# Kernel tuning notes

Hardware: AMD Instinct MI355X
Metric: run time of the kernel (lower is better)

## Reference

```python
import jax, jax.numpy as jnp
import numpy as np

NUM_USERS, NUM_ITEMS = 100000, 50000
N_NODES = NUM_USERS + NUM_ITEMS
N_EDGES = 4_000_000
H = 64
BATCH = 100000
MLP_HIDDEN = 32
N_LAYERS = 3


def setup_inputs() -> dict:
    key = jax.random.key(0)
    ks = jax.random.split(key, 12)
    return {
        "edge_index": jax.random.randint(ks[0], (2, N_EDGES), 0, N_NODES, dtype=jnp.int32),
        "user_ids": jax.random.randint(ks[1], (BATCH,), 0, NUM_USERS, dtype=jnp.int32),
        "item_ids": jax.random.randint(ks[2], (BATCH,), 0, NUM_ITEMS, dtype=jnp.int32),
        "user_emb": jax.random.normal(ks[3], (NUM_USERS, H), jnp.float32),
        "item_emb": jax.random.normal(ks[4], (NUM_ITEMS, H), jnp.float32),
        "Wl": jax.random.normal(ks[5], (N_LAYERS, H, H), jnp.float32) * (1.0 / jnp.sqrt(H)),
        "bl": jnp.zeros((N_LAYERS, H), jnp.float32),
        "Wr": jax.random.normal(ks[6], (N_LAYERS, H, H), jnp.float32) * (1.0 / jnp.sqrt(H)),
        "W1": jax.random.normal(ks[7], (2 * H, MLP_HIDDEN), jnp.float32) * (1.0 / jnp.sqrt(2.0 * H)),
        "b1": jnp.zeros((MLP_HIDDEN,), jnp.float32),
        "W2": jax.random.normal(ks[8], (MLP_HIDDEN, 1), jnp.float32) * (1.0 / jnp.sqrt(1.0 * MLP_HIDDEN)),
        "b2": jnp.zeros((1,), jnp.float32),
    }


def _sage_layer(x, src, dst, Wl_i, bl_i, Wr_i):
    # PyG SAGEConv, mean aggr: out = lin_l(mean_{j in N(i)} x_j) + lin_r(x_i)
    msg = x[src]                                                  # [E, H] gather
    summed = jax.ops.segment_sum(msg, dst, num_segments=N_NODES)  # [N, H] scatter-add
    cnt = jax.ops.segment_sum(jnp.ones((src.shape[0],), x.dtype), dst, num_segments=N_NODES)
    mean = summed / jnp.maximum(cnt, 1.0)[:, None]                # empty neighborhoods -> 0
    return mean @ Wl_i + bl_i + x @ Wr_i


def reference(edge_index, user_ids, item_ids, user_emb, item_emb, Wl, bl, Wr, W1, b1, W2, b2):
    src, dst = edge_index[0], edge_index[1]
    x = jnp.concatenate([user_emb, item_emb], axis=0)  # [N, H]
    for l in range(N_LAYERS):
        x = jax.nn.relu(_sage_layer(x, src, dst, Wl[l], bl[l], Wr[l]))
        # dropout is identity in eval mode
    ue = x[user_ids]                   # [B, H]
    ie = x[item_ids + NUM_USERS]       # [B, H]
    pair = jnp.concatenate([ue, ie], axis=-1)  # [B, 2H]
    h = jax.nn.relu(pair @ W1 + b1)
    rating = (h @ W2 + b2)[:, 0]
    return jnp.clip(rating, 1.0, 5.0)
```

## Files before the change

### kernel.cpp

```cpp
#include <hip/hip_runtime.h>
#include <hip/hip_bf16.h>

#define NUM_USERS 100000
#define NUM_ITEMS 50000
#define N_NODES   150000
#define N_EDGES   4000000
#define H         64
#define BATCH     100000
#define MLP_HIDDEN 32
#define NBUCK     586
#define BCAP      8192
#define ZROW      N_NODES

typedef unsigned short ushort_t;
typedef float f32x2 __attribute__((ext_vector_type(2)));

__device__ __forceinline__ ushort_t f2bf(float f) {
    unsigned u = __float_as_uint(f);
    u = u + 0x7FFFu + ((u >> 16) & 1u);
    return (ushort_t)(u >> 16);
}
__device__ __forceinline__ float bfLO(unsigned u) { return __uint_as_float(u << 16); }
__device__ __forceinline__ float bfHI(unsigned u) { return __uint_as_float(u & 0xFFFF0000u); }

__global__ __launch_bounds__(256) void init_kernel(const float* __restrict__ ue,
                                                   const float* __restrict__ ie,
                                                   ushort_t* __restrict__ xh) {
    int i = blockIdx.x * 256 + threadIdx.x;
    const int UN4 = NUM_USERS * H / 4;
    float4 v = (i < UN4) ? ((const float4*)ue)[i] : ((const float4*)ie)[i - UN4];
    uint2 p;
    p.x = (unsigned)f2bf(v.x) | ((unsigned)f2bf(v.y) << 16);
    p.y = (unsigned)f2bf(v.z) | ((unsigned)f2bf(v.w) << 16);
    ((uint2*)xh)[i] = p;
}

#define SCHUNK 4096
#define SPT    (SCHUNK / 256)
__global__ __launch_bounds__(256) void bucket_scatter_kernel(const int* __restrict__ src,
                                                             const int* __restrict__ dst,
                                                             int* __restrict__ bucketCnt,
                                                             int* __restrict__ ebuf) {
    __shared__ int      histL[NBUCK];
    __shared__ int      startL[NBUCK];
    __shared__ int      adjL[NBUCK];
    __shared__ int      curL[NBUCK];
    __shared__ unsigned staged[SCHUNK];
    __shared__ ushort_t sbuck[SCHUNK];

    int t = threadIdx.x;
    int base = blockIdx.x * SCHUNK;
    int nst = min(SCHUNK, N_EDGES - base);

    for (int i = t; i < NBUCK; i += 256) histL[i] = 0;
    __syncthreads();

    int myd[SPT], mys[SPT];
#pragma unroll
    for (int k = 0; k < SPT; ++k) {
        int e = base + k * 256 + t;
        int d = (e < N_EDGES) ? dst[e] : -1;
        mys[k] = (e < N_EDGES) ? src[e] : 0;
        myd[k] = d;
        if (d >= 0) atomicAdd(&histL[d >> 8], 1);
    }
    __syncthreads();

    if (t < 64) {
        const int CH = (NBUCK + 63) / 64;
        int s0 = t * CH;
        int s1 = min(s0 + CH, NBUCK);
        int s = 0;
        for (int i = s0; i < s1; ++i) s += histL[i];
        int v = s;
#pragma unroll
        for (int off = 1; off < 64; off <<= 1) {
            int u = __shfl_up(v, off, 64);
            if (t >= off) v += u;
        }
        int run = v - s;
        for (int i = s0; i < s1; ++i) {
            startL[i] = run;
            run += histL[i];
        }
    }
    __syncthreads();

    for (int b = t; b < NBUCK; b += 256) {
        int h = histL[b];
        int res = h ? (b * BCAP + atomicAdd(&bucketCnt[b], h)) : 0;
        adjL[b] = res - startL[b];
        curL[b] = startL[b];
    }
    __syncthreads();

#pragma unroll
    for (int k = 0; k < SPT; ++k) {
        int d = myd[k];
        if (d >= 0) {
            int b = d >> 8;
            int pos = atomicAdd(&curL[b], 1);
            staged[pos] = ((unsigned)mys[k] << 8) | (unsigned)(d & 255);
            sbuck[pos] = (ushort_t)b;
        }
    }
    __syncthreads();

    for (int i = t; i < nst; i += 256) {
        int b = sbuck[i];
        ebuf[adjL[b] + i] = (int)staged[i];
    }
}

__global__ __launch_bounds__(512) void bucket_build_kernel(const int* __restrict__ ebuf,
                                                           const int* __restrict__ bucketCnt,
                                                           int* __restrict__ deg,
                                                           int* __restrict__ offsets,
                                                           int* __restrict__ csr) {
    __shared__ int degL[256];
    __shared__ int scanL[256];
    __shared__ int curL[256];
    int t = threadIdx.x;
    int b = blockIdx.x;
    int nodeBase = b << 8;
    int start = b * BCAP;
    int cnt = bucketCnt[b];

    if (t < 256) degL[t] = 0;
    __syncthreads();
    for (int i = t; i < cnt; i += 512)
        atomicAdd(&degL[ebuf[start + i] & 255], 1);
    __syncthreads();

    int v  = (t < 256) ? degL[t] : 0;
    int vp = (v + 3) & ~3;
    if (t < 256) scanL[t] = vp;
    __syncthreads();
#pragma unroll
    for (int off = 1; off < 256; off <<= 1) {
        int u = (t >= off && t < 256) ? scanL[t - off] : 0;
        __syncthreads();
        if (t < 256) scanL[t] += u;
        __syncthreads();
    }

    int excl = 0;
    if (t < 256) {
        excl = scanL[t] - vp;
        int node = nodeBase + t;
        if (node < N_NODES) {
            deg[node] = v;
            offsets[node] = start + excl;
        }
        curL[t] = excl;
    }
    __syncthreads();

    for (int i = t; i < cnt; i += 512) {
        unsigned p = (unsigned)ebuf[start + i];
        int pos = atomicAdd(&curL[p & 255u], 1);
        csr[start + pos] = (int)(p >> 8);
    }
    __syncthreads();

    if (t < 256) {
        for (int i = excl + v; i < excl + vp; ++i) csr[start + i] = ZROW;
    }
}

__global__ __launch_bounds__(256, 8) void gather_mean_kernel(const ushort_t* __restrict__ xh,
                                                             ushort_t* __restrict__ mean_bf,
                                                             const int* __restrict__ offsets,
                                                             const int* __restrict__ deg,
                                                             const int* __restrict__ csr) {
    int slot = threadIdx.x >> 6;
    int lane = threadIdx.x & 63;
    int q    = lane >> 4;
    int fp   = lane & 15;
    int node = blockIdx.x * 4 + slot;

    int base = offsets[node];
    int cnt  = deg[node];
    int cnt4 = (cnt + 3) & ~3;
    const uint2* xr = (const uint2*)xh;

    float a0 = 0.f, a1 = 0.f, a2 = 0.f, a3 = 0.f;

    for (int c = 0; c < cnt4; c += 64) {
        int rem = cnt4 - c;
        int sid = (lane < rem) ? csr[base + c + lane] : ZROW;
        int nq = min(64, rem) >> 2;
#define PROC(JJ) { int s = __shfl(sid, 4 * (JJ) + q, 64);                 \
        uint2 u = xr[s * 16 + fp];                                        \
        a0 += bfLO(u.x); a1 += bfHI(u.x); a2 += bfLO(u.y); a3 += bfHI(u.y); }
        int j = 0;
        for (; j + 2 <= nq; j += 2) { PROC(j) PROC(j + 1) }
        for (; j < nq; ++j) { PROC(j) }
#undef PROC
    }

    a0 += __shfl_xor(a0, 16, 64); a1 += __shfl_xor(a1, 16, 64);
    a2 += __shfl_xor(a2, 16, 64); a3 += __shfl_xor(a3, 16, 64);
    a0 += __shfl_xor(a0, 32, 64); a1 += __shfl_xor(a1, 32, 64);
    a2 += __shfl_xor(a2, 32, 64); a3 += __shfl_xor(a3, 32, 64);

    if (lane < 16) {
        float rc = 1.0f / fmaxf((float)cnt, 1.0f);
        uint2 p;
        p.x = (unsigned)f2bf(a0 * rc) | ((unsigned)f2bf(a1 * rc) << 16);
        p.y = (unsigned)f2bf(a2 * rc) | ((unsigned)f2bf(a3 * rc) << 16);
        *(uint2*)&mean_bf[node * H + fp * 4] = p;
    }
}

__global__ __launch_bounds__(256) void transform_kernel(ushort_t* __restrict__ xh,
                                                        const ushort_t* __restrict__ mean_bf,
                                                        const float* __restrict__ Wl,
                                                        const float* __restrict__ bl,
                                                        const float* __restrict__ Wr) {
    __shared__ float    sWl[H * H];
    __shared__ float    sWr[H * H];
    __shared__ unsigned sMT[H / 2][128];
    __shared__ unsigned sXT[H / 2][128];

    int t = threadIdx.x;
    int node0 = blockIdx.x * 128;

    for (int i = t; i < H * H / 4; i += 256) {
        ((float4*)sWl)[i] = ((const float4*)Wl)[i];
        ((float4*)sWr)[i] = ((const float4*)Wr)[i];
    }
#pragma unroll
    for (int it = 0; it < 8; ++it) {
        int idx = it * 256 + t;
        int n = idx & 127;
        int qd = idx >> 7;
        int node = node0 + n;
        uint2 mu = make_uint2(0u, 0u);
        uint2 xu = make_uint2(0u, 0u);
        if (node < N_NODES) {
            mu = *(const uint2*)&mean_bf[node * H + qd * 4];
            xu = *(const uint2*)&xh[node * H + qd * 4];
        }
        sMT[qd * 2][n]     = mu.x;
        sMT[qd * 2 + 1][n] = mu.y;
        sXT[qd * 2][n]     = xu.x;
        sXT[qd * 2 + 1][n] = xu.y;
    }
    __syncthreads();

    int tx = t & 7;
    int ty = t >> 3;
    int nbase = node0 + ty * 4;

    f32x2 acc[4][4];
#pragma unroll
    for (int j = 0; j < 4; ++j)
#pragma unroll
        for (int p = 0; p < 4; ++p) acc[j][p] = (f32x2)(0.0f);

    for (int kp = 0; kp < H / 2; ++kp) {
        uint4 mu = *(const uint4*)&sMT[kp][ty * 4];
        uint4 xu = *(const uint4*)&sXT[kp][ty * 4];
        int k0 = kp * 2;
        float4 wl00 = *(const float4*)&sWl[k0 * H + tx * 8];
        float4 wl01 = *(const float4*)&sWl[k0 * H + tx * 8 + 4];
        float4 wr00 = *(const float4*)&sWr[k0 * H + tx * 8];
        float4 wr01 = *(const float4*)&sWr[k0 * H + tx * 8 + 4];
        float4 wl10 = *(const float4*)&sWl[(k0 + 1) * H + tx * 8];
        float4 wl11 = *(const float4*)&sWl[(k0 + 1) * H + tx * 8 + 4];
        float4 wr10 = *(const float4*)&sWr[(k0 + 1) * H + tx * 8];
        float4 wr11 = *(const float4*)&sWr[(k0 + 1) * H + tx * 8 + 4];
        f32x2 wl0p[4] = {{wl00.x, wl00.y}, {wl00.z, wl00.w}, {wl01.x, wl01.y}, {wl01.z, wl01.w}};
        f32x2 wr0p[4] = {{wr00.x, wr00.y}, {wr00.z, wr00.w}, {wr01.x, wr01.y}, {wr01.z, wr01.w}};
        f32x2 wl1p[4] = {{wl10.x, wl10.y}, {wl10.z, wl10.w}, {wl11.x, wl11.y}, {wl11.z, wl11.w}};
        f32x2 wr1p[4] = {{wr10.x, wr10.y}, {wr10.z, wr10.w}, {wr11.x, wr11.y}, {wr11.z, wr11.w}};
        const unsigned mua[4] = {mu.x, mu.y, mu.z, mu.w};
        const unsigned xua[4] = {xu.x, xu.y, xu.z, xu.w};
#pragma unroll
        for (int j = 0; j < 4; ++j) {
            f32x2 m0 = (f32x2)(bfLO(mua[j]));
            f32x2 m1 = (f32x2)(bfHI(mua[j]));
            f32x2 x0 = (f32x2)(bfLO(xua[j]));
            f32x2 x1 = (f32x2)(bfHI(xua[j]));
#pragma unroll
            for (int p = 0; p < 4; ++p) {
                f32x2 a = acc[j][p];
                a = __builtin_elementwise_fma(m0, wl0p[p], a);
                a = __builtin_elementwise_fma(x0, wr0p[p], a);
                a = __builtin_elementwise_fma(m1, wl1p[p], a);
                a = __builtin_elementwise_fma(x1, wr1p[p], a);
                acc[j][p] = a;
            }
        }
    }

    float4 b0 = *(const float4*)&bl[tx * 8];
    float4 b1 = *(const float4*)&bl[tx * 8 + 4];
    f32x2 bias[4] = {{b0.x, b0.y}, {b0.z, b0.w}, {b1.x, b1.y}, {b1.z, b1.w}};
#pragma unroll
    for (int j = 0; j < 4; ++j) {
        int node = nbase + j;
        if (node < N_NODES) {
            uint4 pk;
            unsigned w[4];
#pragma unroll
            for (int p = 0; p < 4; ++p) {
                float o0 = fmaxf(acc[j][p].x + bias[p].x, 0.0f);
                float o1 = fmaxf(acc[j][p].y + bias[p].y, 0.0f);
                w[p] = (unsigned)f2bf(o0) | ((unsigned)f2bf(o1) << 16);
            }
            pk.x = w[0]; pk.y = w[1]; pk.z = w[2]; pk.w = w[3];
            *(uint4*)&xh[node * H + tx * 8] = pk;
        }
    }
}

__global__ __launch_bounds__(256) void mlp_kernel(const ushort_t* __restrict__ xh,
                                                  const int* __restrict__ uids,
                                                  const int* __restrict__ iids,
                                                  const float* __restrict__ W1,
                                                  const float* __restrict__ b1,
                                                  const float* __restrict__ W2,
                                                  const float* __restrict__ b2,
                                                  float* __restrict__ out) {
    __shared__ float sW1[2 * H * MLP_HIDDEN];
    __shared__ float sPair[8][2 * H];
    __shared__ float sW2[MLP_HIDDEN];

    for (int i = threadIdx.x; i < 2 * H * MLP_HIDDEN; i += 256) sW1[i] = W1[i];
    if (threadIdx.x < MLP_HIDDEN) sW2[threadIdx.x] = W2[threadIdx.x];

    int slot = threadIdx.x >> 5;
    int j    = threadIdx.x & 31;
    int b = blockIdx.x * 8 + slot;

    int u  = uids[b];
    int it = iids[b] + NUM_USERS;
    const uint2* xr = (const uint2*)xh;
    uint2 v = (j < 16) ? xr[u * 16 + j] : xr[it * 16 + (j - 16)];
    int off = (j < 16) ? j * 4 : (H + (j - 16) * 4);
    sPair[slot][off + 0] = bfLO(v.x);
    sPair[slot][off + 1] = bfHI(v.x);
    sPair[slot][off + 2] = bfLO(v.y);
    sPair[slot][off + 3] = bfHI(v.y);
    __syncthreads();

    float hacc = b1[j];
#pragma unroll
    for (int k = 0; k < 2 * H; ++k)
        hacc = fmaf(sPair[slot][k], sW1[k * MLP_HIDDEN + j], hacc);
    hacc = fmaxf(hacc, 0.0f);

    float r = hacc * sW2[j];
#pragma unroll
    for (int off2 = 16; off2; off2 >>= 1) r += __shfl_down(r, off2, 32);

    if (j == 0) out[b] = fminf(fmaxf(r + b2[0], 1.0f), 5.0f);
}

extern "C" void kernel_launch(void* const* d_in, const int* in_sizes, int n_in,
                              void* d_out, int out_size, void* d_ws, size_t ws_size,
                              hipStream_t stream) {
    const int*   edge_index = (const int*)d_in[0];
    const int*   user_ids   = (const int*)d_in[1];
    const int*   item_ids   = (const int*)d_in[2];
    const float* user_emb   = (const float*)d_in[3];
    const float* item_emb   = (const float*)d_in[4];
    const float* Wl         = (const float*)d_in[5];
    const float* bl         = (const float*)d_in[6];
    const float* Wr         = (const float*)d_in[7];
    const float* W1         = (const float*)d_in[8];
    const float* b1         = (const float*)d_in[9];
    const float* W2         = (const float*)d_in[10];
    const float* b2         = (const float*)d_in[11];
    float* out = (float*)d_out;

    const int* src = edge_index;
    const int* dst = edge_index + N_EDGES;

    const size_t NH = (size_t)N_NODES * H;
    ushort_t* xh      = (ushort_t*)d_ws;
    int* ebuf         = (int*)(xh + NH + H);
    ushort_t* mean_bf = (ushort_t*)ebuf;
    int* deg          = ebuf + (size_t)NBUCK * BCAP;
    int* offsets      = deg + N_NODES;
    int* bucketCnt    = offsets + N_NODES;
    int* csr          = bucketCnt + NBUCK;

    init_kernel<<<(N_NODES * H / 4) / 256, 256, 0, stream>>>(user_emb, item_emb, xh);
    hipMemsetAsync(xh + NH, 0, H * sizeof(ushort_t), stream);

    hipMemsetAsync(bucketCnt, 0, NBUCK * sizeof(int), stream);
    bucket_scatter_kernel<<<(N_EDGES + SCHUNK - 1) / SCHUNK, 256, 0, stream>>>(
        src, dst, bucketCnt, ebuf);
    bucket_build_kernel<<<NBUCK, 512, 0, stream>>>(ebuf, bucketCnt, deg, offsets, csr);

    const int TGRID = (N_NODES + 127) / 128;
    for (int l = 0; l < 3; ++l) {
        gather_mean_kernel<<<N_NODES / 4, 256, 0, stream>>>(xh, mean_bf, offsets, deg, csr);
        transform_kernel<<<TGRID, 256, 0, stream>>>(
            xh, mean_bf, Wl + (size_t)l * H * H, bl + (size_t)l * H,
            Wr + (size_t)l * H * H);
    }

    mlp_kernel<<<BATCH / 8, 256, 0, stream>>>(xh, user_ids, item_ids, W1, b1, W2, b2, out);
}
```

Before: 489.9 us.

## Tile MLP over 128 pairs, store weights as bf16, widen bucket build

Rewrites the final MLP kernel to process 128 user-item pairs per block as a register-tiled GEMM with W1 held in shared memory as bf16. This amortizes the per-block weight load, which was previously repeated for every 8 pairs. The SAGE transform kernel also stores Wl/Wr as bf16 in shared memory to halve LDS traffic and footprint. The bucket build kernel now uses 1024 threads. Weight rounding to bf16 adds numerical error.

```diff
diff --git a/kernel.cpp b/kernel.cpp
--- a/kernel.cpp
+++ b/kernel.cpp
@@ -20,6 +20,9 @@
     u = u + 0x7FFFu + ((u >> 16) & 1u);
     return (ushort_t)(u >> 16);
 }
+__device__ __forceinline__ unsigned pk2bf(float a, float b) {
+    return (unsigned)f2bf(a) | ((unsigned)f2bf(b) << 16);
+}
 __device__ __forceinline__ float bfLO(unsigned u) { return __uint_as_float(u << 16); }
 __device__ __forceinline__ float bfHI(unsigned u) { return __uint_as_float(u & 0xFFFF0000u); }
 
@@ -30,8 +33,8 @@
     const int UN4 = NUM_USERS * H / 4;
     float4 v = (i < UN4) ? ((const float4*)ue)[i] : ((const float4*)ie)[i - UN4];
     uint2 p;
-    p.x = (unsigned)f2bf(v.x) | ((unsigned)f2bf(v.y) << 16);
-    p.y = (unsigned)f2bf(v.z) | ((unsigned)f2bf(v.w) << 16);
+    p.x = pk2bf(v.x, v.y);
+    p.y = pk2bf(v.z, v.w);
     ((uint2*)xh)[i] = p;
 }
 
@@ -112,11 +115,11 @@
     }
 }
 
-__global__ __launch_bounds__(512) void bucket_build_kernel(const int* __restrict__ ebuf,
-                                                           const int* __restrict__ bucketCnt,
-                                                           int* __restrict__ deg,
-                                                           int* __restrict__ offsets,
-                                                           int* __restrict__ csr) {
+__global__ __launch_bounds__(1024) void bucket_build_kernel(const int* __restrict__ ebuf,
+                                                            const int* __restrict__ bucketCnt,
+                                                            int* __restrict__ deg,
+                                                            int* __restrict__ offsets,
+                                                            int* __restrict__ csr) {
     __shared__ int degL[256];
     __shared__ int scanL[256];
     __shared__ int curL[256];
@@ -128,7 +131,7 @@
 
     if (t < 256) degL[t] = 0;
     __syncthreads();
-    for (int i = t; i < cnt; i += 512)
+    for (int i = t; i < cnt; i += 1024)
         atomicAdd(&degL[ebuf[start + i] & 255], 1);
     __syncthreads();
 
@@ -156,7 +159,7 @@
     }
     __syncthreads();
 
-    for (int i = t; i < cnt; i += 512) {
+    for (int i = t; i < cnt; i += 1024) {
         unsigned p = (unsigned)ebuf[start + i];
         int pos = atomicAdd(&curL[p & 255u], 1);
         csr[start + pos] = (int)(p >> 8);
@@ -207,8 +210,8 @@
     if (lane < 16) {
         float rc = 1.0f / fmaxf((float)cnt, 1.0f);
         uint2 p;
-        p.x = (unsigned)f2bf(a0 * rc) | ((unsigned)f2bf(a1 * rc) << 16);
-        p.y = (unsigned)f2bf(a2 * rc) | ((unsigned)f2bf(a3 * rc) << 16);
+        p.x = pk2bf(a0 * rc, a1 * rc);
+        p.y = pk2bf(a2 * rc, a3 * rc);
         *(uint2*)&mean_bf[node * H + fp * 4] = p;
     }
 }
@@ -218,8 +221,8 @@
                                                         const float* __restrict__ Wl,
                                                         const float* __restrict__ bl,
                                                         const float* __restrict__ Wr) {
-    __shared__ float    sWl[H * H];
-    __shared__ float    sWr[H * H];
+    __shared__ unsigned sWlh[H * H / 2];
+    __shared__ unsigned sWrh[H * H / 2];
     __shared__ unsigned sMT[H / 2][128];
     __shared__ unsigned sXT[H / 2][128];
 
@@ -227,8 +230,10 @@
     int node0 = blockIdx.x * 128;
 
     for (int i = t; i < H * H / 4; i += 256) {
-        ((float4*)sWl)[i] = ((const float4*)Wl)[i];
-        ((float4*)sWr)[i] = ((const float4*)Wr)[i];
+        float4 a = ((const float4*)Wl)[i];
+        float4 b = ((const float4*)Wr)[i];
+        ((uint2*)sWlh)[i] = make_uint2(pk2bf(a.x, a.y), pk2bf(a.z, a.w));
+        ((uint2*)sWrh)[i] = make_uint2(pk2bf(b.x, b.y), pk2bf(b.z, b.w));
     }
 #pragma unroll
     for (int it = 0; it < 8; ++it) {
@@ -263,18 +268,22 @@
         uint4 mu = *(const uint4*)&sMT[kp][ty * 4];
         uint4 xu = *(const uint4*)&sXT[kp][ty * 4];
         int k0 = kp * 2;
-        float4 wl00 = *(const float4*)&sWl[k0 * H + tx * 8];
-        float4 wl01 = *(const float4*)&sWl[k0 * H + tx * 8 + 4];
-        float4 wr00 = *(const float4*)&sWr[k0 * H + tx * 8];
-        float4 wr01 = *(const float4*)&sWr[k0 * H + tx * 8 + 4];
-        float4 wl10 = *(const float4*)&sWl[(k0 + 1) * H + tx * 8];
-        float4 wl11 = *(const float4*)&sWl[(k0 + 1) * H + tx * 8 + 4];
-        float4 wr10 = *(const float4*)&sWr[(k0 + 1) * H + tx * 8];
-        float4 wr11 = *(const float4*)&sWr[(k0 + 1) * H + tx * 8 + 4];
-        f32x2 wl0p[4] = {{wl00.x, wl00.y}, {wl00.z, wl00.w}, {wl01.x, wl01.y}, {wl01.z, wl01.w}};
-        f32x2 wr0p[4] = {{wr00.x, wr00.y}, {wr00.z, wr00.w}, {wr01.x, wr01.y}, {wr01.z, wr01.w}};
-        f32x2 wl1p[4] = {{wl10.x, wl10.y}, {wl10.z, wl10.w}, {wl11.x, wl11.y}, {wl11.z, wl11.w}};
-        f32x2 wr1p[4] = {{wr10.x, wr10.y}, {wr10.z, wr10.w}, {wr11.x, wr11.y}, {wr11.z, wr11.w}};
+        uint4 wl0u = *(const uint4*)&sWlh[k0 * (H / 2) + tx * 4];
+        uint4 wl1u = *(const uint4*)&sWlh[(k0 + 1) * (H / 2) + tx * 4];
+        uint4 wr0u = *(const uint4*)&sWrh[k0 * (H / 2) + tx * 4];
+        uint4 wr1u = *(const uint4*)&sWrh[(k0 + 1) * (H / 2) + tx * 4];
+        const unsigned wl0a[4] = {wl0u.x, wl0u.y, wl0u.z, wl0u.w};
+        const unsigned wl1a[4] = {wl1u.x, wl1u.y, wl1u.z, wl1u.w};
+        const unsigned wr0a[4] = {wr0u.x, wr0u.y, wr0u.z, wr0u.w};
+        const unsigned wr1a[4] = {wr1u.x, wr1u.y, wr1u.z, wr1u.w};
+        f32x2 wl0p[4], wl1p[4], wr0p[4], wr1p[4];
+#pragma unroll
+        for (int p = 0; p < 4; ++p) {
+            wl0p[p] = (f32x2){bfLO(wl0a[p]), bfHI(wl0a[p])};
+            wl1p[p] = (f32x2){bfLO(wl1a[p]), bfHI(wl1a[p])};
+            wr0p[p] = (f32x2){bfLO(wr0a[p]), bfHI(wr0a[p])};
+            wr1p[p] = (f32x2){bfLO(wr1a[p]), bfHI(wr1a[p])};
+        }
         const unsigned mua[4] = {mu.x, mu.y, mu.z, mu.w};
         const unsigned xua[4] = {xu.x, xu.y, xu.z, xu.w};
 #pragma unroll
@@ -308,7 +317,7 @@
             for (int p = 0; p < 4; ++p) {
                 float o0 = fmaxf(acc[j][p].x + bias[p].x, 0.0f);
                 float o1 = fmaxf(acc[j][p].y + bias[p].y, 0.0f);
-                w[p] = (unsigned)f2bf(o0) | ((unsigned)f2bf(o1) << 16);
+                w[p] = pk2bf(o0, o1);
             }
             pk.x = w[0]; pk.y = w[1]; pk.z = w[2]; pk.w = w[3];
             *(uint4*)&xh[node * H + tx * 8] = pk;
@@ -324,39 +333,102 @@
                                                   const float* __restrict__ W2,
                                                   const float* __restrict__ b2,
                                                   float* __restrict__ out) {
-    __shared__ float sW1[2 * H * MLP_HIDDEN];
-    __shared__ float sPair[8][2 * H];
-    __shared__ float sW2[MLP_HIDDEN];
-
-    for (int i = threadIdx.x; i < 2 * H * MLP_HIDDEN; i += 256) sW1[i] = W1[i];
-    if (threadIdx.x < MLP_HIDDEN) sW2[threadIdx.x] = W2[threadIdx.x];
-
-    int slot = threadIdx.x >> 5;
-    int j    = threadIdx.x & 31;
-    int b = blockIdx.x * 8 + slot;
-
-    int u  = uids[b];
-    int it = iids[b] + NUM_USERS;
+    __shared__ unsigned sW1h[2 * H * MLP_HIDDEN / 2];
+    __shared__ unsigned sPT[H][128];
+    __shared__ float    sW2f[MLP_HIDDEN];
+    __shared__ float    sB1f[MLP_HIDDEN];
+    __shared__ int      sUid[128];
+    __shared__ int      sIid[128];
+
+    int t = threadIdx.x;
+    int item0 = blockIdx.x * 128;
+
+    for (int i = t; i < 2 * H * MLP_HIDDEN / 4; i += 256) {
+        float4 a = ((const float4*)W1)[i];
+        ((uint2*)sW1h)[i] = make_uint2(pk2bf(a.x, a.y), pk2bf(a.z, a.w));
+    }
+    if (t < MLP_HIDDEN) {
+        sW2f[t] = W2[t];
+        sB1f[t] = b1[t];
+    }
+    if (t < 128) {
+        int g = item0 + t;
+        sUid[t] = (g < BATCH) ? uids[g] : 0;
+        sIid[t] = (g < BATCH) ? iids[g] : 0;
+    }
+    __syncthreads();
+
     const uint2* xr = (const uint2*)xh;
-    uint2 v = (j < 16) ? xr[u * 16 + j] : xr[it * 16 + (j - 16)];
-    int off = (j < 16) ? j * 4 : (H + (j - 16) * 4);
-    sPair[slot][off + 0] = bfLO(v.x);
-    sPair[slot][off + 1] = bfHI(v.x);
-    sPair[slot][off + 2] = bfLO(v.y);
-    sPair[slot][off + 3] = bfHI(v.y);
-    __syncthreads();
-
-    float hacc = b1[j];
-#pragma unroll
-    for (int k = 0; k < 2 * H; ++k)
-        hacc = fmaf(sPair[slot][k], sW1[k * MLP_HIDDEN + j], hacc);
-    hacc = fmaxf(hacc, 0.0f);
-
-    float r = hacc * sW2[j];
-#pragma unroll
-    for (int off2 = 16; off2; off2 >>= 1) r += __shfl_down(r, off2, 32);
-
-    if (j == 0) out[b] = fminf(fmaxf(r + b2[0], 1.0f), 5.0f);
+#pragma unroll
+    for (int it = 0; it < 16; ++it) {
+        int idx = it * 256 + t;
+        int item = idx & 127;
+        int chunk = idx >> 7;
+        int half = chunk >> 4;
+        int fq = chunk & 15;
+        int row = half ? (sIid[item] + NUM_USERS) : sUid[item];
+        uint2 v = xr[row * 16 + fq];
+        int kp0 = half * 32 + fq * 2;
+        sPT[kp0][item]     = v.x;
+        sPT[kp0 + 1][item] = v.y;
+    }
+    __syncthreads();
+
+    int tx = t & 3;
+    int ty = t >> 2;
+    int ibase = item0 + ty * 2;
+
+    f32x2 acc[2][4];
+#pragma unroll
+    for (int j = 0; j < 2; ++j)
+#pragma unroll
+        for (int p = 0; p < 4; ++p) acc[j][p] = (f32x2)(0.0f);
+
+    for (int kp = 0; kp < H; ++kp) {
+        uint2 pv = *(const uint2*)&sPT[kp][ty * 2];
+        int k0 = kp * 2;
+        uint4 w0u = *(const uint4*)&sW1h[k0 * (MLP_HIDDEN / 2) + tx * 4];
+        uint4 w1u = *(const uint4*)&sW1h[(k0 + 1) * (MLP_HIDDEN / 2) + tx * 4];
+        const unsigned w0a[4] = {w0u.x, w0u.y, w0u.z, w0u.w};
+        const unsigned w1a[4] = {w1u.x, w1u.y, w1u.z, w1u.w};
+        f32x2 w0p[4], w1p[4];
+#pragma unroll
+        for (int p = 0; p < 4; ++p) {
+            w0p[p] = (f32x2){bfLO(w0a[p]), bfHI(w0a[p])};
+            w1p[p] = (f32x2){bfLO(w1a[p]), bfHI(w1a[p])};
+        }
+        const unsigned pva[2] = {pv.x, pv.y};
+#pragma unroll
+        for (int j = 0; j < 2; ++j) {
+            f32x2 m0 = (f32x2)(bfLO(pva[j]));
+            f32x2 m1 = (f32x2)(bfHI(pva[j]));
+#pragma unroll
+            for (int p = 0; p < 4; ++p) {
+                f32x2 a = acc[j][p];
+                a = __builtin_elementwise_fma(m0, w0p[p], a);
+                a = __builtin_elementwise_fma(m1, w1p[p], a);
+                acc[j][p] = a;
+            }
+        }
+    }
+
+    float b2v = b2[0];
+#pragma unroll
+    for (int j = 0; j < 2; ++j) {
+        float partial = 0.0f;
+#pragma unroll
+        for (int p = 0; p < 4; ++p) {
+            float h0 = fmaxf(acc[j][p].x + sB1f[tx * 8 + p * 2],     0.0f);
+            float h1 = fmaxf(acc[j][p].y + sB1f[tx * 8 + p * 2 + 1], 0.0f);
+            partial = fmaf(h0, sW2f[tx * 8 + p * 2],     partial);
+            partial = fmaf(h1, sW2f[tx * 8 + p * 2 + 1], partial);
+        }
+        partial += __shfl_xor(partial, 1, 64);
+        partial += __shfl_xor(partial, 2, 64);
+        int g = ibase + j;
+        if (tx == 0 && g < BATCH)
+            out[g] = fminf(fmaxf(partial + b2v, 1.0f), 5.0f);
+    }
 }
 
 extern "C" void kernel_launch(void* const* d_in, const int* in_sizes, int n_in,
@@ -394,7 +466,7 @@
     hipMemsetAsync(bucketCnt, 0, NBUCK * sizeof(int), stream);
     bucket_scatter_kernel<<<(N_EDGES + SCHUNK - 1) / SCHUNK, 256, 0, stream>>>(
         src, dst, bucketCnt, ebuf);
-    bucket_build_kernel<<<NBUCK, 512, 0, stream>>>(ebuf, bucketCnt, deg, offsets, csr);
+    bucket_build_kernel<<<NBUCK, 1024, 0, stream>>>(ebuf, bucketCnt, deg, offsets, csr);
 
     const int TGRID = (N_NODES + 127) / 128;
     for (int l = 0; l < 3; ++l) {
@@ -404,5 +476,6 @@
             Wr + (size_t)l * H * H);
     }
 
-    mlp_kernel<<<BATCH / 8, 256, 0, stream>>>(xh, user_ids, item_ids, W1, b1, W2, b2, out);
-}
+    mlp_kernel<<<(BATCH + 127) / 128, 256, 0, stream>>>(xh, user_ids, item_ids,
+                                                        W1, b1, W2, b2, out);
+}
```

Measured after the change: 487.5 us. Within noise of the previous version (-0.5%).
